# Kernel optimization log

Measured on AMD Instinct MI355X. Metric: run time of the kernel, lower is better.

## Reference

```python
import jax, jax.numpy as jnp
import numpy as np

U, I, D = 100000, 50000, 64
N = U + I
E_G, E_U, E_I = 2400000, 1600000, 800000


def _spmm(rows, cols, vals, x, n):
    # sparse [n, m] @ dense [m, d] via gather + scale + segment-sum scatter
    return jax.ops.segment_sum(x[cols] * vals[:, None], rows, num_segments=n)


def setup_inputs() -> dict:
    key = jax.random.key(0)
    ks = jax.random.split(key, 11)
    return {
        "user_emb": jax.random.normal(ks[0], (U, D), dtype=jnp.float32),
        "item_emb": jax.random.normal(ks[1], (I, D), dtype=jnp.float32),
        "graph_rows": jax.random.randint(ks[2], (E_G,), 0, N, dtype=jnp.int32),
        "graph_cols": jax.random.randint(ks[3], (E_G,), 0, N, dtype=jnp.int32),
        "graph_vals": jax.random.uniform(ks[4], (E_G,), dtype=jnp.float32),
        "user_rows": jax.random.randint(ks[5], (E_U,), 0, U, dtype=jnp.int32),
        "user_cols": jax.random.randint(ks[6], (E_U,), 0, U, dtype=jnp.int32),
        "user_vals": jax.random.uniform(ks[7], (E_U,), dtype=jnp.float32),
        "item_rows": jax.random.randint(ks[8], (E_I,), 0, I, dtype=jnp.int32),
        "item_cols": jax.random.randint(ks[9], (E_I,), 0, I, dtype=jnp.int32),
        "item_vals": jax.random.uniform(ks[10], (E_I,), dtype=jnp.float32),
    }


def reference(user_emb, item_emb,
              graph_rows, graph_cols, graph_vals,
              user_rows, user_cols, user_vals,
              item_rows, item_cols, item_vals):
    all_emb = jnp.concatenate([user_emb, item_emb], axis=0)  # [N, D]
    all_emb1 = _spmm(graph_rows, graph_cols, graph_vals, all_emb, N)
    user_emb2 = _spmm(user_rows, user_cols, user_vals, user_emb, U)
    item_emb2 = _spmm(item_rows, item_cols, item_vals, item_emb, I)
    user_emb1, item_emb1 = all_emb1[:U], all_emb1[U:]
    return (user_emb1, item_emb1, user_emb2, item_emb2)
```

## Files before the change

kernel.cpp:

```cpp
#include <hip/hip_runtime.h>

#define DDIM 64
constexpr int U_CNT = 100000;
constexpr int I_CNT = 50000;
constexpr int N_CNT = U_CNT + I_CNT;
constexpr int NB    = N_CNT + U_CNT + I_CNT;

constexpr int BIN_ROWS_LOG = 8;
constexpr int BIN_ROWS = 1 << BIN_ROWS_LOG;
constexpr int BINS = (NB + BIN_ROWS - 1) / BIN_ROWS;
constexpr int BINS_PAD = 1536;
constexpr int SORT_EDGES = 4096;
constexpr int HIST_EDGES = 16384;
constexpr int CAP = 4672;
constexpr int NSLOT = 10;

constexpr int SB_LOG = 12;
constexpr int NSB = (NB + (1 << SB_LOG) - 1) >> SB_LOG;
constexpr int NSB_PAD = 128;
constexpr int BWIN = 48;

typedef unsigned u32x2 __attribute__((ext_vector_type(2)));
typedef unsigned u32x4 __attribute__((ext_vector_type(4)));

__device__ __forceinline__ int wave_incl_scan(int v, int lane) {
#pragma unroll
    for (int off = 1; off < 64; off <<= 1) {
        int t = __shfl_up(v, off, 64);
        if (lane >= off) v += t;
    }
    return v;
}

__device__ __forceinline__ unsigned short f2bf_rne(float f) {
    unsigned u = __float_as_uint(f);
    unsigned r = (u + 0x7FFFu + ((u >> 16) & 1u)) >> 16;
    return (unsigned short)r;
}

__global__ __launch_bounds__(256) void convert_emb(const float* __restrict__ ue,
                                                   const float* __restrict__ ie,
                                                   unsigned short* __restrict__ emb16) {
    int g = blockIdx.x * 256 + threadIdx.x;
    constexpr int UG = U_CNT * (DDIM / 4);
    constexpr int TG = N_CNT * (DDIM / 4);
    if (g >= TG) return;
    float4 v = (g < UG) ? ((const float4*)ue)[g] : ((const float4*)ie)[g - UG];
    ushort4 o;
    o.x = f2bf_rne(v.x); o.y = f2bf_rne(v.y); o.z = f2bf_rne(v.z); o.w = f2bf_rne(v.w);
    ((ushort4*)emb16)[g] = o;
}

__global__ __launch_bounds__(1024) void hist_conv(const int* __restrict__ gr,
                                                  const int* __restrict__ ur,
                                                  const int* __restrict__ ir,
                                                  int EG, int EU, int EI,
                                                  int* __restrict__ cnt,
                                                  const float* __restrict__ ue,
                                                  const float* __restrict__ ie,
                                                  unsigned short* __restrict__ emb16) {
    __shared__ int h[BINS_PAD];
    for (int i = threadIdx.x; i < BINS_PAD; i += 1024) h[i] = 0;

    if (emb16) {
        constexpr int UG = U_CNT * (DDIM / 4);
        constexpr int TG = N_CNT * (DDIM / 4);
        int stride = (int)gridDim.x * 1024;
        for (int g = blockIdx.x * 1024 + threadIdx.x; g < TG; g += stride) {
            float4 v = (g < UG) ? ((const float4*)ue)[g] : ((const float4*)ie)[g - UG];
            ushort4 o;
            o.x = f2bf_rne(v.x); o.y = f2bf_rne(v.y); o.z = f2bf_rne(v.z); o.w = f2bf_rne(v.w);
            ((ushort4*)emb16)[g] = o;
        }
    }
    __syncthreads();

    int base = blockIdx.x * HIST_EDGES;
    int Et = EG + EU + EI;
    for (int j = 0; j < HIST_EDGES / 1024; ++j) {
        int e = base + j * 1024 + threadIdx.x;
        if (e < Et) {
            int b;
            if (e < EG)           b = gr[e];
            else if (e < EG + EU) b = N_CNT + ur[e - EG];
            else                  b = N_CNT + U_CNT + ir[e - EG - EU];
            atomicAdd(&h[b >> BIN_ROWS_LOG], 1);
        }
    }
    __syncthreads();
    for (int i = threadIdx.x; i < BINS; i += 1024) {
        int v = h[i];
        if (v) atomicAdd(&cnt[i], v);
    }
}

__global__ __launch_bounds__(1024) void scan_bins(const int* __restrict__ cnt,
                                                  int* __restrict__ bin_base,
                                                  int* __restrict__ bin_cursor,
                                                  int* __restrict__ sb_base,
                                                  int* __restrict__ sb_cursor,
                                                  int E_total) {
    __shared__ int wsum[16], woff[16];
    int tid = threadIdx.x, lane = tid & 63, wid = tid >> 6;
    int i0 = 2 * tid, i1 = 2 * tid + 1;
    int c0 = (i0 < BINS) ? cnt[i0] : 0;
    int c1 = (i1 < BINS) ? cnt[i1] : 0;
    int v = c0 + c1;
    int incl = wave_incl_scan(v, lane);
    if (lane == 63) wsum[wid] = incl;
    __syncthreads();
    if (wid == 0 && lane < 16) {
        int s = wsum[lane], si = s;
#pragma unroll
        for (int off = 1; off < 16; off <<= 1) {
            int t = __shfl_up(si, off, 64);
            if (lane >= off) si += t;
        }
        woff[lane] = si - s;
    }
    __syncthreads();
    int e = incl - v + woff[wid];
    if (i0 < BINS) { bin_base[i0] = e;      bin_cursor[i0] = e; }
    if (i1 < BINS) { bin_base[i1] = e + c0; bin_cursor[i1] = e + c0; }
    if (tid == 0) bin_base[BINS] = E_total;
    if (sb_base) {
        __syncthreads();
        if (tid <= NSB) {
            int idx = tid << (SB_LOG - BIN_ROWS_LOG);
            int vv = (idx >= BINS) ? E_total : bin_base[idx];
            sb_base[tid] = vv;
            if (tid < NSB) sb_cursor[tid] = vv;
        }
    }
}

__global__ __launch_bounds__(512, 6) void sbsort_all(
        const int* __restrict__ gr, const int* __restrict__ gc, const float* __restrict__ gv,
        const int* __restrict__ ur, const int* __restrict__ uc, const float* __restrict__ uv,
        const int* __restrict__ ir, const int* __restrict__ ic, const float* __restrict__ iv,
        int EG, int EU, int EI,
        int* __restrict__ sb_cursor, uint2* __restrict__ poolA) {
    __shared__ uint2 sorted[SORT_EDGES];
    __shared__ unsigned char ssb[SORT_EDGES];
    __shared__ int hist[NSB_PAD];
    __shared__ int lscan[NSB_PAD];
    __shared__ int lcur[NSB_PAD];
    __shared__ int wsum2[2];

    int tid = threadIdx.x, lane = tid & 63, wid = tid >> 6;
    for (int i = tid; i < NSB_PAD; i += 512) { hist[i] = 0; lcur[i] = 0; }
    __syncthreads();

    const int Et = EG + EU + EI;
    int start = blockIdx.x * SORT_EDGES;
    int base_e = start + tid * 8;
    int myb[8]; unsigned mylo[8]; float myv[8];

#pragma unroll
    for (int j = 0; j < 8; j += 4) {
        int e = base_e + j;
        int sg0 = (e < EG) ? 0 : (e < EG + EU ? 1 : 2);
        int sg3 = (e + 3 < EG) ? 0 : (e + 3 < EG + EU ? 1 : 2);
        if (e + 3 < Et && sg0 == sg3) {
            const int* R; const int* Cc; const float* V; int boff, goff, loc;
            if (sg0 == 0)      { R = gr; Cc = gc; V = gv; boff = 0;             goff = 0;     loc = e; }
            else if (sg0 == 1) { R = ur; Cc = uc; V = uv; boff = N_CNT;         goff = 0;     loc = e - EG; }
            else               { R = ir; Cc = ic; V = iv; boff = N_CNT + U_CNT; goff = U_CNT; loc = e - EG - EU; }
            int4   r4 = *(const int4*)(R + loc);
            int4   c4 = *(const int4*)(Cc + loc);
            float4 v4 = *(const float4*)(V + loc);
            int rr[4] = {r4.x, r4.y, r4.z, r4.w};
            int cc[4] = {c4.x, c4.y, c4.z, c4.w};
            float vv[4] = {v4.x, v4.y, v4.z, v4.w};
#pragma unroll
            for (int q = 0; q < 4; ++q) {
                int bucket = boff + rr[q];
                int sb = bucket >> SB_LOG;
                myb[j + q] = sb;
                mylo[j + q] = ((unsigned)(bucket & 4095) << 18) | (unsigned)(goff + cc[q]);
                myv[j + q] = vv[q];
                atomicAdd(&hist[sb], 1);
            }
        } else {
#pragma unroll
            for (int q = 0; q < 4; ++q) {
                int ee = e + q;
                if (ee < Et) {
                    int r, c; float vl; int boff, goff;
                    if (ee < EG)           { r = gr[ee]; c = gc[ee]; vl = gv[ee]; boff = 0; goff = 0; }
                    else if (ee < EG + EU) { int k = ee - EG;      r = ur[k]; c = uc[k]; vl = uv[k]; boff = N_CNT;         goff = 0; }
                    else                   { int k = ee - EG - EU; r = ir[k]; c = ic[k]; vl = iv[k]; boff = N_CNT + U_CNT; goff = U_CNT; }
                    int bucket = boff + r;
                    int sb = bucket >> SB_LOG;
                    myb[j + q] = sb;
                    mylo[j + q] = ((unsigned)(bucket & 4095) << 18) | (unsigned)(goff + c);
                    myv[j + q] = vl;
                    atomicAdd(&hist[sb], 1);
                } else myb[j + q] = -1;
            }
        }
    }
    __syncthreads();

    int v = 0, incl = 0;
    if (tid < NSB_PAD) {
        v = hist[tid];
        incl = wave_incl_scan(v, lane);
        if (lane == 63) wsum2[wid] = incl;
    }
    __syncthreads();
    if (tid < NSB_PAD) {
        int st = incl - v + (wid ? wsum2[0] : 0);
        lscan[tid] = st;
        if (tid < NSB && v) hist[tid] = atomicAdd(&sb_cursor[tid], v);
    }
    __syncthreads();

#pragma unroll
    for (int j = 0; j < 8; ++j) {
        if (myb[j] >= 0) {
            int p = lscan[myb[j]] + atomicAdd(&lcur[myb[j]], 1);
            sorted[p] = make_uint2(mylo[j], __float_as_uint(myv[j]));
            ssb[p] = (unsigned char)myb[j];
        }
    }
    __syncthreads();

    int cntE = min(SORT_EDGES, Et - start);
    for (int pos = tid; pos < cntE; pos += 512) {
        int b = ssb[pos];
        uint2 t = sorted[pos];
        u32x2 q; q.x = t.x; q.y = t.y;
        __builtin_nontemporal_store(q, (u32x2*)&poolA[hist[b] + (pos - lscan[b])]);
    }
}

__global__ __launch_bounds__(512, 6) void binsort2(const uint2* __restrict__ poolA,
                                                   const int* __restrict__ sb_base, int Et,
                                                   int* __restrict__ bin_cursor,
                                                   uint2* __restrict__ poolB) {
    __shared__ uint2 sorted[SORT_EDGES];
    __shared__ unsigned char sbin[SORT_EDGES];
    __shared__ int hist[BWIN];
    __shared__ int lscan[BWIN];
    __shared__ int lcur[BWIN];
    __shared__ int ssbb[NSB + 1];
    __shared__ int W0s, nloc;

    int tid = threadIdx.x, lane = tid & 63;
    if (tid < BWIN) { hist[tid] = 0; }
    if (tid <= NSB) ssbb[tid] = sb_base[tid];
    __syncthreads();

    int start = blockIdx.x * SORT_EDGES;
    int base_e = start + tid * 8;
    int sb;
    {
        int lo2 = 0, hi2 = NSB - 1;
        while (lo2 < hi2) {
            int mid = (lo2 + hi2 + 1) >> 1;
            if (ssbb[mid] <= base_e) lo2 = mid; else hi2 = mid - 1;
        }
        sb = lo2;
    }
    if (tid == 0) W0s = sb << (SB_LOG - BIN_ROWS_LOG);
    __syncthreads();
    int W0 = W0s;

    int myb[8]; uint2 myp[8];
#pragma unroll
    for (int j = 0; j < 8; j += 2) {
        int e = base_e + j;
        uint2 p0, p1;
        bool v1 = (e + 1 < Et), v0 = (e < Et);
        if (v1) {
            u32x4 q = __builtin_nontemporal_load((const u32x4*)(poolA + e));
            p0.x = q.x; p0.y = q.y; p1.x = q.z; p1.y = q.w;
        } else if (v0) {
            u32x2 q = __builtin_nontemporal_load((const u32x2*)(poolA + e));
            p0.x = q.x; p0.y = q.y;
        }
        if (v0) {
            while (sb < NSB - 1 && e >= ssbb[sb + 1]) ++sb;
            int b = (sb << (SB_LOG - BIN_ROWS_LOG)) + (int)(p0.x >> 26);
            int slot = b - W0;
            if ((unsigned)slot < (unsigned)BWIN) {
                myb[j] = slot; myp[j] = p0;
                atomicAdd(&hist[slot], 1);
            } else {
                int gp = atomicAdd(&bin_cursor[b], 1);
                poolB[gp] = p0;
                myb[j] = -1;
            }
        } else myb[j] = -1;
        if (v1) {
            int e1 = e + 1;
            while (sb < NSB - 1 && e1 >= ssbb[sb + 1]) ++sb;
            int b = (sb << (SB_LOG - BIN_ROWS_LOG)) + (int)(p1.x >> 26);
            int slot = b - W0;
            if ((unsigned)slot < (unsigned)BWIN) {
                myb[j + 1] = slot; myp[j + 1] = p1;
                atomicAdd(&hist[slot], 1);
            } else {
                int gp = atomicAdd(&bin_cursor[b], 1);
                poolB[gp] = p1;
                myb[j + 1] = -1;
            }
        } else myb[j + 1] = -1;
    }
    __syncthreads();

    if (tid < 64) {
        int vv = (tid < BWIN) ? hist[tid] : 0;
        int incl = wave_incl_scan(vv, lane);
        if (tid < BWIN) { lscan[tid] = incl - vv; lcur[tid] = incl - vv; }
        if (tid == BWIN - 1) nloc = incl;
    }
    __syncthreads();
    if (tid < BWIN && hist[tid] > 0)
        hist[tid] = atomicAdd(&bin_cursor[W0 + tid], hist[tid]);
    __syncthreads();

#pragma unroll
    for (int j = 0; j < 8; ++j) {
        if (myb[j] >= 0) {
            int p = atomicAdd(&lcur[myb[j]], 1);
            sorted[p] = myp[j];
            sbin[p] = (unsigned char)myb[j];
        }
    }
    __syncthreads();

    int tot = nloc;
    for (int pos = tid; pos < tot; pos += 512) {
        int sl = sbin[pos];
        uint2 t = sorted[pos];
        u32x2 q; q.x = t.x; q.y = t.y;
        __builtin_nontemporal_store(q, (u32x2*)&poolB[hist[sl] + (pos - lscan[sl])]);
    }
}

__global__ __launch_bounds__(512) void binsort(const int* __restrict__ rows,
                                               const int* __restrict__ cols,
                                               const float* __restrict__ vals, int E,
                                               int bucket_base, int gidx_base,
                                               int* __restrict__ bin_cursor,
                                               uint2* __restrict__ pool) {
    __shared__ uint2 sorted[SORT_EDGES];
    __shared__ unsigned short sbin[SORT_EDGES];
    __shared__ int hist[BINS_PAD];
    __shared__ int lscan[BINS_PAD];
    __shared__ int lcur[BINS_PAD];
    __shared__ int wsum[8], woff[8];

    int tid = threadIdx.x, lane = tid & 63, wid = tid >> 6;
    for (int i = tid; i < BINS_PAD; i += 512) { hist[i] = 0; lcur[i] = 0; }
    __syncthreads();

    int start = blockIdx.x * SORT_EDGES;
    int base_e = start + tid * 8;
    int myb[8]; unsigned mylo[8]; float myv[8];
#pragma unroll
    for (int j = 0; j < 8; j += 4) {
        int e = base_e + j;
        if (e + 3 < E) {
            int4   r4 = *(const int4*)(rows + e);
            int4   c4 = *(const int4*)(cols + e);
            float4 v4 = *(const float4*)(vals + e);
            int rr[4] = {r4.x, r4.y, r4.z, r4.w};
            int cc[4] = {c4.x, c4.y, c4.z, c4.w};
            float vv[4] = {v4.x, v4.y, v4.z, v4.w};
#pragma unroll
            for (int q = 0; q < 4; ++q) {
                int bucket = bucket_base + rr[q];
                myb[j + q] = bucket >> BIN_ROWS_LOG;
                mylo[j + q] = ((unsigned)(bucket & (BIN_ROWS - 1)) << 18) |
                              (unsigned)(gidx_base + cc[q]);
                myv[j + q] = vv[q];
                atomicAdd(&hist[myb[j + q]], 1);
            }
        } else {
#pragma unroll
            for (int q = 0; q < 4; ++q) {
                int ee = e + q;
                if (ee < E) {
                    int bucket = bucket_base + rows[ee];
                    myb[j + q] = bucket >> BIN_ROWS_LOG;
                    mylo[j + q] = ((unsigned)(bucket & (BIN_ROWS - 1)) << 18) |
                                  (unsigned)(gidx_base + cols[ee]);
                    myv[j + q] = vals[ee];
                    atomicAdd(&hist[myb[j + q]], 1);
                } else myb[j + q] = -1;
            }
        }
    }
    __syncthreads();

    int s0 = 3 * tid, s1 = s0 + 1, s2 = s0 + 2;
    int h0 = hist[s0], h1 = hist[s1], h2 = hist[s2];
    int v = h0 + h1 + h2;
    int incl = wave_incl_scan(v, lane);
    if (lane == 63) wsum[wid] = incl;
    __syncthreads();
    if (wid == 0 && lane < 8) {
        int s = wsum[lane], si = s;
#pragma unroll
        for (int off = 1; off < 8; off <<= 1) {
            int t = __shfl_up(si, off, 64);
            if (lane >= off) si += t;
        }
        woff[lane] = si - s;
    }
    __syncthreads();
    int e0 = incl - v + woff[wid];
    lscan[s0] = e0; lscan[s1] = e0 + h0; lscan[s2] = e0 + h0 + h1;
    if (s0 < BINS && h0) hist[s0] = atomicAdd(&bin_cursor[s0], h0);
    if (s1 < BINS && h1) hist[s1] = atomicAdd(&bin_cursor[s1], h1);
    if (s2 < BINS && h2) hist[s2] = atomicAdd(&bin_cursor[s2], h2);
    __syncthreads();

#pragma unroll
    for (int j = 0; j < 8; ++j) {
        if (myb[j] >= 0) {
            int p = lscan[myb[j]] + atomicAdd(&lcur[myb[j]], 1);
            sorted[p] = make_uint2(mylo[j], __float_as_uint(myv[j]));
            sbin[p] = (unsigned short)myb[j];
        }
    }
    __syncthreads();

    int cntE = min(SORT_EDGES, E - start);
    for (int pos = tid; pos < cntE; pos += 512) {
        int b = sbin[pos];
        pool[hist[b] + (pos - lscan[b])] = sorted[pos];
    }
}

template <bool BF16>
__global__ __launch_bounds__(512, 8) void refine_accum(const int* __restrict__ bin_base,
                                                       const uint2* __restrict__ pool,
                                                       const unsigned short* __restrict__ emb16,
                                                       const float* __restrict__ ue,
                                                       const float* __restrict__ ie,
                                                       float* __restrict__ out) {
    __shared__ uint2 sorted[CAP];
    __shared__ int rhist[BIN_ROWS];
    __shared__ int rstart[BIN_ROWS];
    __shared__ int rcur[BIN_ROWS];
    __shared__ int wsum[4];
    int tid = threadIdx.x, lane = tid & 63, wid = tid >> 6;
    int b = blockIdx.x;
    int s = bin_base[b], e = bin_base[b + 1];
    int cnt = min(e - s, CAP);

    if (tid < BIN_ROWS) rhist[tid] = 0;
    __syncthreads();

    uint2 my[NSLOT];
    const u32x2* poolv = (const u32x2*)(pool + s);
#pragma unroll
    for (int j = 0; j < NSLOT; ++j) {
        int idx = tid + j * 512;
        if (idx < cnt) {
            u32x2 q = __builtin_nontemporal_load(poolv + idx);
            my[j].x = q.x; my[j].y = q.y;
            atomicAdd(&rhist[(q.x >> 18) & 255u], 1);
        }
    }
    __syncthreads();

    int v = 0, incl = 0;
    if (tid < BIN_ROWS) {
        v = rhist[tid];
        incl = wave_incl_scan(v, lane);
        if (lane == 63) wsum[wid] = incl;
    }
    __syncthreads();
    if (tid < BIN_ROWS) {
        int off = 0;
#pragma unroll
        for (int w = 0; w < 4; ++w)
            if (w < wid) off += wsum[w];
        int st = incl - v + off;
        rstart[tid] = st; rcur[tid] = st;
    }
    __syncthreads();

#pragma unroll
    for (int j = 0; j < NSLOT; ++j) {
        int idx = tid + j * 512;
        if (idx < cnt) {
            int pos = atomicAdd(&rcur[(my[j].x >> 18) & 255u], 1);
            sorted[pos] = my[j];
        }
    }
    __syncthreads();

    long long rowbase = (long long)b * BIN_ROWS;
    auto gather = [&](unsigned gi) -> float {
        if (BF16) return __uint_as_float((unsigned)emb16[(gi << 6) + lane] << 16);
        return (gi < (unsigned)U_CNT) ? ue[((size_t)gi << 6) + lane]
                                      : ie[(((size_t)gi - U_CNT) << 6) + lane];
    };
    for (int r = wid; r < BIN_ROWS; r += 8) {
        long long row = rowbase + r;
        if (row >= NB) break;
        int k = rstart[r], ke = k + rhist[r];
        float acc0 = 0.f, acc1 = 0.f;
        for (; k + 8 <= ke; k += 8) {
            uint2 p0 = sorted[k],     p1 = sorted[k + 1], p2 = sorted[k + 2], p3 = sorted[k + 3];
            uint2 p4 = sorted[k + 4], p5 = sorted[k + 5], p6 = sorted[k + 6], p7 = sorted[k + 7];
            float x0 = gather(p0.x & 0x3FFFFu);
            float x1 = gather(p1.x & 0x3FFFFu);
            float x2 = gather(p2.x & 0x3FFFFu);
            float x3 = gather(p3.x & 0x3FFFFu);
            float x4 = gather(p4.x & 0x3FFFFu);
            float x5 = gather(p5.x & 0x3FFFFu);
            float x6 = gather(p6.x & 0x3FFFFu);
            float x7 = gather(p7.x & 0x3FFFFu);
            acc0 += __uint_as_float(p0.y) * x0;
            acc1 += __uint_as_float(p1.y) * x1;
            acc0 += __uint_as_float(p2.y) * x2;
            acc1 += __uint_as_float(p3.y) * x3;
            acc0 += __uint_as_float(p4.y) * x4;
            acc1 += __uint_as_float(p5.y) * x5;
            acc0 += __uint_as_float(p6.y) * x6;
            acc1 += __uint_as_float(p7.y) * x7;
        }
        for (; k + 4 <= ke; k += 4) {
            uint2 p0 = sorted[k], p1 = sorted[k + 1], p2 = sorted[k + 2], p3 = sorted[k + 3];
            float x0 = gather(p0.x & 0x3FFFFu);
            float x1 = gather(p1.x & 0x3FFFFu);
            float x2 = gather(p2.x & 0x3FFFFu);
            float x3 = gather(p3.x & 0x3FFFFu);
            acc0 += __uint_as_float(p0.y) * x0;
            acc1 += __uint_as_float(p1.y) * x1;
            acc0 += __uint_as_float(p2.y) * x2;
            acc1 += __uint_as_float(p3.y) * x3;
        }
        for (; k < ke; ++k) {
            uint2 p = sorted[k];
            acc0 += __uint_as_float(p.y) * gather(p.x & 0x3FFFFu);
        }
        __builtin_nontemporal_store(acc0 + acc1, &out[(size_t)row * DDIM + lane]);
    }
}

__global__ void spmm_graph_kernel(const int* __restrict__ rows, const int* __restrict__ cols,
                                  const float* __restrict__ vals,
                                  const float* __restrict__ user_emb,
                                  const float* __restrict__ item_emb,
                                  float* __restrict__ out, int E) {
    long long idx = (long long)blockIdx.x * blockDim.x + threadIdx.x;
    int e = (int)(idx >> 6), d = (int)(idx & 63);
    if (e >= E) return;
    int r = rows[e], c = cols[e];
    float v = vals[e];
    float x = (c < U_CNT) ? user_emb[(long long)c * DDIM + d]
                          : item_emb[(long long)(c - U_CNT) * DDIM + d];
    atomicAdd(&out[(long long)r * DDIM + d], v * x);
}

__global__ void spmm_plain_kernel(const int* __restrict__ rows, const int* __restrict__ cols,
                                  const float* __restrict__ vals,
                                  const float* __restrict__ emb,
                                  float* __restrict__ out, int E) {
    long long idx = (long long)blockIdx.x * blockDim.x + threadIdx.x;
    int e = (int)(idx >> 6), d = (int)(idx & 63);
    if (e >= E) return;
    int r = rows[e], c = cols[e];
    atomicAdd(&out[(long long)r * DDIM + d], vals[e] * emb[(long long)c * DDIM + d]);
}

extern "C" void kernel_launch(void* const* d_in, const int* in_sizes, int n_in,
                              void* d_out, int out_size, void* d_ws, size_t ws_size,
                              hipStream_t stream) {
    const float* user_emb = (const float*)d_in[0];
    const float* item_emb = (const float*)d_in[1];
    const int*   g_rows   = (const int*)d_in[2];
    const int*   g_cols   = (const int*)d_in[3];
    const float* g_vals   = (const float*)d_in[4];
    const int*   u_rows   = (const int*)d_in[5];
    const int*   u_cols   = (const int*)d_in[6];
    const float* u_vals   = (const float*)d_in[7];
    const int*   i_rows   = (const int*)d_in[8];
    const int*   i_cols   = (const int*)d_in[9];
    const float* i_vals   = (const float*)d_in[10];
    float* out = (float*)d_out;

    const int EG = in_sizes[2];
    const int EU = in_sizes[5];
    const int EI = in_sizes[8];
    const int Et = EG + EU + EI;

    const size_t emb_bytes = (size_t)N_CNT * DDIM * sizeof(unsigned short);

    size_t t_off_bb   = (size_t)BINS_PAD * sizeof(int);
    size_t t_off_bc   = t_off_bb + (size_t)(BINS + 1) * sizeof(int);
    size_t t_off_sbb  = t_off_bc + (size_t)BINS * sizeof(int);
    size_t t_off_sbc  = t_off_sbb + (size_t)(NSB + 1) * sizeof(int);
    size_t t_off_pa   = (t_off_sbc + (size_t)NSB * sizeof(int) + 15) & ~(size_t)15;
    size_t t_off_pb   = t_off_pa + (size_t)Et * sizeof(uint2);
    size_t needed_2p  = t_off_pb + (size_t)Et * sizeof(uint2);
    size_t t_off_emb  = (needed_2p + 15) & ~(size_t)15;
    size_t needed_na  = t_off_emb + emb_bytes;
    bool pa_fits_emb  = (size_t)Et * sizeof(uint2) >= emb_bytes;

    size_t o_off_base   = (size_t)BINS_PAD * sizeof(int);
    size_t o_off_cursor = o_off_base + (size_t)(BINS + 1) * sizeof(int);
    size_t o_off_pool   = (o_off_cursor + (size_t)BINS * sizeof(int) + 15) & ~(size_t)15;
    size_t o_off_emb    = o_off_pool + (size_t)Et * sizeof(uint2);
    size_t needed_min   = o_off_emb;
    size_t needed_full  = o_off_emb + emb_bytes;

    if (ws_size >= needed_2p && pa_fits_emb) {
        bool noalias = (ws_size >= needed_na);
        int*   cnt        = (int*)d_ws;
        int*   bin_base   = (int*)((char*)d_ws + t_off_bb);
        int*   bin_cursor = (int*)((char*)d_ws + t_off_bc);
        int*   sb_base    = (int*)((char*)d_ws + t_off_sbb);
        int*   sb_cursor  = (int*)((char*)d_ws + t_off_sbc);
        uint2* poolA      = (uint2*)((char*)d_ws + t_off_pa);
        uint2* poolB      = (uint2*)((char*)d_ws + t_off_pb);
        unsigned short* emb16 = noalias ? (unsigned short*)((char*)d_ws + t_off_emb)
                                        : (unsigned short*)poolA;

        hipMemsetAsync(cnt, 0, (size_t)BINS_PAD * sizeof(int), stream);

        unsigned hblocks = (unsigned)((Et + HIST_EDGES - 1) / HIST_EDGES);
        hist_conv<<<hblocks, 1024, 0, stream>>>(g_rows, u_rows, i_rows, EG, EU, EI, cnt,
                                                user_emb, item_emb,
                                                noalias ? emb16 : (unsigned short*)nullptr);
        scan_bins<<<1, 1024, 0, stream>>>(cnt, bin_base, bin_cursor, sb_base, sb_cursor, Et);

        unsigned nb2 = (unsigned)((Et + SORT_EDGES - 1) / SORT_EDGES);
        sbsort_all<<<nb2, 512, 0, stream>>>(g_rows, g_cols, g_vals,
                                            u_rows, u_cols, u_vals,
                                            i_rows, i_cols, i_vals,
                                            EG, EU, EI, sb_cursor, poolA);
        binsort2<<<nb2, 512, 0, stream>>>(poolA, sb_base, Et, bin_cursor, poolB);

        if (!noalias) {
            unsigned cgrid = (unsigned)((N_CNT * (DDIM / 4) + 255) / 256);
            convert_emb<<<cgrid, 256, 0, stream>>>(user_emb, item_emb, emb16);
        }

        refine_accum<true><<<BINS, 512, 0, stream>>>(bin_base, poolB, emb16,
                                                     user_emb, item_emb, out);
    } else if (ws_size >= needed_min) {
        int*   cnt        = (int*)d_ws;
        int*   bin_base   = (int*)((char*)d_ws + o_off_base);
        int*   bin_cursor = (int*)((char*)d_ws + o_off_cursor);
        uint2* pool       = (uint2*)((char*)d_ws + o_off_pool);
        unsigned short* emb16 = (unsigned short*)((char*)d_ws + o_off_emb);
        bool use_bf16 = (ws_size >= needed_full);

        hipMemsetAsync(cnt, 0, (size_t)BINS_PAD * sizeof(int), stream);

        unsigned hblocks = (unsigned)((Et + HIST_EDGES - 1) / HIST_EDGES);
        hist_conv<<<hblocks, 1024, 0, stream>>>(g_rows, u_rows, i_rows, EG, EU, EI, cnt,
                                                user_emb, item_emb,
                                                use_bf16 ? emb16 : (unsigned short*)nullptr);
        scan_bins<<<1, 1024, 0, stream>>>(cnt, bin_base, bin_cursor, nullptr, nullptr, Et);

        unsigned gb = (unsigned)((EG + SORT_EDGES - 1) / SORT_EDGES);
        unsigned ub = (unsigned)((EU + SORT_EDGES - 1) / SORT_EDGES);
        unsigned ib = (unsigned)((EI + SORT_EDGES - 1) / SORT_EDGES);
        binsort<<<gb, 512, 0, stream>>>(g_rows, g_cols, g_vals, EG, 0,             0,     bin_cursor, pool);
        binsort<<<ub, 512, 0, stream>>>(u_rows, u_cols, u_vals, EU, N_CNT,         0,     bin_cursor, pool);
        binsort<<<ib, 512, 0, stream>>>(i_rows, i_cols, i_vals, EI, N_CNT + U_CNT, U_CNT, bin_cursor, pool);

        if (use_bf16)
            refine_accum<true><<<BINS, 512, 0, stream>>>(bin_base, pool, emb16,
                                                         user_emb, item_emb, out);
        else
            refine_accum<false><<<BINS, 512, 0, stream>>>(bin_base, pool, (const unsigned short*)nullptr,
                                                          user_emb, item_emb, out);
    } else {
        hipMemsetAsync(d_out, 0, (size_t)out_size * sizeof(float), stream);
        const int block = 256;
        {
            long long t = (long long)EG * DDIM;
            spmm_graph_kernel<<<(unsigned)((t + block - 1) / block), block, 0, stream>>>(
                g_rows, g_cols, g_vals, user_emb, item_emb, out, EG);
        }
        {
            long long t = (long long)EU * DDIM;
            spmm_plain_kernel<<<(unsigned)((t + block - 1) / block), block, 0, stream>>>(
                u_rows, u_cols, u_vals, user_emb, out + (size_t)N_CNT * DDIM, EU);
        }
        {
            long long t = (long long)EI * DDIM;
            spmm_plain_kernel<<<(unsigned)((t + block - 1) / block), block, 0, stream>>>(
                i_rows, i_cols, i_vals, item_emb, out + (size_t)(N_CNT + U_CNT) * DDIM, EI);
        }
    }
}
```

Before: 357.0 us.

## Halve bin size and gather bf16 pairs with half-wave edge split in accumulate

Bins now hold 128 rows instead of 256. The refine kernel drops to 256 threads with a smaller LDS buffer and higher occupancy, and the second-level sort window grows to 80 slots using a two-wave scan. In the accumulate loop each half-wave handles a different edge and loads 32-bit pairs of bf16 values, then the two halves are combined with a cross-half shuffle and written as float2. This aims to cut LDS pressure and use wider gather loads per lane. The fallback one-pass sort path and the fp32 gather path are removed, so small workspaces now go to the naive kernels.

Result: no change. 355.4 us (-0.4%).

```diff
diff --git a/kernel.cpp b/kernel.cpp
--- a/kernel.cpp
+++ b/kernel.cpp
@@ -6,22 +6,24 @@
 constexpr int N_CNT = U_CNT + I_CNT;
 constexpr int NB    = N_CNT + U_CNT + I_CNT;
 
-constexpr int BIN_ROWS_LOG = 8;
+constexpr int BIN_ROWS_LOG = 7;
 constexpr int BIN_ROWS = 1 << BIN_ROWS_LOG;
 constexpr int BINS = (NB + BIN_ROWS - 1) / BIN_ROWS;
-constexpr int BINS_PAD = 1536;
+constexpr int BINS_PAD = 2560;
 constexpr int SORT_EDGES = 4096;
 constexpr int HIST_EDGES = 16384;
-constexpr int CAP = 4672;
+constexpr int CAP = 2432;
 constexpr int NSLOT = 10;
 
 constexpr int SB_LOG = 12;
 constexpr int NSB = (NB + (1 << SB_LOG) - 1) >> SB_LOG;
 constexpr int NSB_PAD = 128;
-constexpr int BWIN = 48;
+constexpr int BWIN = 80;
+constexpr int BWIN_PAD = 128;
 
 typedef unsigned u32x2 __attribute__((ext_vector_type(2)));
 typedef unsigned u32x4 __attribute__((ext_vector_type(4)));
+typedef float    f32x2 __attribute__((ext_vector_type(2)));
 
 __device__ __forceinline__ int wave_incl_scan(int v, int lane) {
 #pragma unroll
@@ -102,10 +104,11 @@
                                                   int E_total) {
     __shared__ int wsum[16], woff[16];
     int tid = threadIdx.x, lane = tid & 63, wid = tid >> 6;
-    int i0 = 2 * tid, i1 = 2 * tid + 1;
+    int i0 = 3 * tid, i1 = i0 + 1, i2 = i0 + 2;
     int c0 = (i0 < BINS) ? cnt[i0] : 0;
     int c1 = (i1 < BINS) ? cnt[i1] : 0;
-    int v = c0 + c1;
+    int c2 = (i2 < BINS) ? cnt[i2] : 0;
+    int v = c0 + c1 + c2;
     int incl = wave_incl_scan(v, lane);
     if (lane == 63) wsum[wid] = incl;
     __syncthreads();
@@ -120,21 +123,20 @@
     }
     __syncthreads();
     int e = incl - v + woff[wid];
-    if (i0 < BINS) { bin_base[i0] = e;      bin_cursor[i0] = e; }
-    if (i1 < BINS) { bin_base[i1] = e + c0; bin_cursor[i1] = e + c0; }
+    if (i0 < BINS) { bin_base[i0] = e;           bin_cursor[i0] = e; }
+    if (i1 < BINS) { bin_base[i1] = e + c0;      bin_cursor[i1] = e + c0; }
+    if (i2 < BINS) { bin_base[i2] = e + c0 + c1; bin_cursor[i2] = e + c0 + c1; }
     if (tid == 0) bin_base[BINS] = E_total;
-    if (sb_base) {
-        __syncthreads();
-        if (tid <= NSB) {
-            int idx = tid << (SB_LOG - BIN_ROWS_LOG);
-            int vv = (idx >= BINS) ? E_total : bin_base[idx];
-            sb_base[tid] = vv;
-            if (tid < NSB) sb_cursor[tid] = vv;
-        }
-    }
-}
-
-__global__ __launch_bounds__(512, 6) void sbsort_all(
+    __syncthreads();
+    if (tid <= NSB) {
+        int idx = tid << (SB_LOG - BIN_ROWS_LOG);
+        int vv = (idx >= BINS) ? E_total : bin_base[idx];
+        sb_base[tid] = vv;
+        if (tid < NSB) sb_cursor[tid] = vv;
+    }
+}
+
+__global__ __launch_bounds__(512, 8) void sbsort_all(
         const int* __restrict__ gr, const int* __restrict__ gc, const float* __restrict__ gv,
         const int* __restrict__ ur, const int* __restrict__ uc, const float* __restrict__ uv,
         const int* __restrict__ ir, const int* __restrict__ ic, const float* __restrict__ iv,
@@ -235,20 +237,21 @@
     }
 }
 
-__global__ __launch_bounds__(512, 6) void binsort2(const uint2* __restrict__ poolA,
+__global__ __launch_bounds__(512, 8) void binsort2(const uint2* __restrict__ poolA,
                                                    const int* __restrict__ sb_base, int Et,
                                                    int* __restrict__ bin_cursor,
                                                    uint2* __restrict__ poolB) {
     __shared__ uint2 sorted[SORT_EDGES];
     __shared__ unsigned char sbin[SORT_EDGES];
-    __shared__ int hist[BWIN];
-    __shared__ int lscan[BWIN];
-    __shared__ int lcur[BWIN];
+    __shared__ int hist[BWIN_PAD];
+    __shared__ int lscan[BWIN_PAD];
+    __shared__ int lcur[BWIN_PAD];
     __shared__ int ssbb[NSB + 1];
-    __shared__ int W0s, nloc;
-
-    int tid = threadIdx.x, lane = tid & 63;
-    if (tid < BWIN) { hist[tid] = 0; }
+    __shared__ int wsum2[2];
+    __shared__ int sblo_s, nloc;
+
+    int tid = threadIdx.x, lane = tid & 63, wid = tid >> 6;
+    if (tid < BWIN_PAD) hist[tid] = 0;
     if (tid <= NSB) ssbb[tid] = sb_base[tid];
     __syncthreads();
 
@@ -263,9 +266,17 @@
         }
         sb = lo2;
     }
-    if (tid == 0) W0s = sb << (SB_LOG - BIN_ROWS_LOG);
-    __syncthreads();
-    int W0 = W0s;
+    if (tid == 0) {
+        int lo2 = 0, hi2 = NSB - 1;
+        while (lo2 < hi2) {
+            int mid = (lo2 + hi2 + 1) >> 1;
+            if (ssbb[mid] <= start) lo2 = mid; else hi2 = mid - 1;
+        }
+        sblo_s = lo2;
+    }
+    __syncthreads();
+    int sb_lo = sblo_s;
+    int W0 = sb_lo << (SB_LOG - BIN_ROWS_LOG);
 
     int myb[8]; uint2 myp[8];
 #pragma unroll
@@ -282,12 +293,12 @@
         }
         if (v0) {
             while (sb < NSB - 1 && e >= ssbb[sb + 1]) ++sb;
-            int b = (sb << (SB_LOG - BIN_ROWS_LOG)) + (int)(p0.x >> 26);
-            int slot = b - W0;
+            int slot = ((sb - sb_lo) << (SB_LOG - BIN_ROWS_LOG)) + (int)(p0.x >> 25);
             if ((unsigned)slot < (unsigned)BWIN) {
                 myb[j] = slot; myp[j] = p0;
                 atomicAdd(&hist[slot], 1);
             } else {
+                int b = (sb << (SB_LOG - BIN_ROWS_LOG)) + (int)(p0.x >> 25);
                 int gp = atomicAdd(&bin_cursor[b], 1);
                 poolB[gp] = p0;
                 myb[j] = -1;
@@ -296,12 +307,12 @@
         if (v1) {
             int e1 = e + 1;
             while (sb < NSB - 1 && e1 >= ssbb[sb + 1]) ++sb;
-            int b = (sb << (SB_LOG - BIN_ROWS_LOG)) + (int)(p1.x >> 26);
-            int slot = b - W0;
+            int slot = ((sb - sb_lo) << (SB_LOG - BIN_ROWS_LOG)) + (int)(p1.x >> 25);
             if ((unsigned)slot < (unsigned)BWIN) {
                 myb[j + 1] = slot; myp[j + 1] = p1;
                 atomicAdd(&hist[slot], 1);
             } else {
+                int b = (sb << (SB_LOG - BIN_ROWS_LOG)) + (int)(p1.x >> 25);
                 int gp = atomicAdd(&bin_cursor[b], 1);
                 poolB[gp] = p1;
                 myb[j + 1] = -1;
@@ -310,11 +321,17 @@
     }
     __syncthreads();
 
-    if (tid < 64) {
-        int vv = (tid < BWIN) ? hist[tid] : 0;
-        int incl = wave_incl_scan(vv, lane);
-        if (tid < BWIN) { lscan[tid] = incl - vv; lcur[tid] = incl - vv; }
-        if (tid == BWIN - 1) nloc = incl;
+    int v = 0, incl = 0;
+    if (tid < BWIN_PAD) {
+        v = hist[tid];
+        incl = wave_incl_scan(v, lane);
+        if (lane == 63) wsum2[wid] = incl;
+    }
+    __syncthreads();
+    if (tid < BWIN_PAD) {
+        int st = incl - v + (wid ? wsum2[0] : 0);
+        lscan[tid] = st; lcur[tid] = st;
+        if (tid == BWIN_PAD - 1) nloc = st + v;
     }
     __syncthreads();
     if (tid < BWIN && hist[tid] > 0)
@@ -340,114 +357,15 @@
     }
 }
 
-__global__ __launch_bounds__(512) void binsort(const int* __restrict__ rows,
-                                               const int* __restrict__ cols,
-                                               const float* __restrict__ vals, int E,
-                                               int bucket_base, int gidx_base,
-                                               int* __restrict__ bin_cursor,
-                                               uint2* __restrict__ pool) {
-    __shared__ uint2 sorted[SORT_EDGES];
-    __shared__ unsigned short sbin[SORT_EDGES];
-    __shared__ int hist[BINS_PAD];
-    __shared__ int lscan[BINS_PAD];
-    __shared__ int lcur[BINS_PAD];
-    __shared__ int wsum[8], woff[8];
-
-    int tid = threadIdx.x, lane = tid & 63, wid = tid >> 6;
-    for (int i = tid; i < BINS_PAD; i += 512) { hist[i] = 0; lcur[i] = 0; }
-    __syncthreads();
-
-    int start = blockIdx.x * SORT_EDGES;
-    int base_e = start + tid * 8;
-    int myb[8]; unsigned mylo[8]; float myv[8];
-#pragma unroll
-    for (int j = 0; j < 8; j += 4) {
-        int e = base_e + j;
-        if (e + 3 < E) {
-            int4   r4 = *(const int4*)(rows + e);
-            int4   c4 = *(const int4*)(cols + e);
-            float4 v4 = *(const float4*)(vals + e);
-            int rr[4] = {r4.x, r4.y, r4.z, r4.w};
-            int cc[4] = {c4.x, c4.y, c4.z, c4.w};
-            float vv[4] = {v4.x, v4.y, v4.z, v4.w};
-#pragma unroll
-            for (int q = 0; q < 4; ++q) {
-                int bucket = bucket_base + rr[q];
-                myb[j + q] = bucket >> BIN_ROWS_LOG;
-                mylo[j + q] = ((unsigned)(bucket & (BIN_ROWS - 1)) << 18) |
-                              (unsigned)(gidx_base + cc[q]);
-                myv[j + q] = vv[q];
-                atomicAdd(&hist[myb[j + q]], 1);
-            }
-        } else {
-#pragma unroll
-            for (int q = 0; q < 4; ++q) {
-                int ee = e + q;
-                if (ee < E) {
-                    int bucket = bucket_base + rows[ee];
-                    myb[j + q] = bucket >> BIN_ROWS_LOG;
-                    mylo[j + q] = ((unsigned)(bucket & (BIN_ROWS - 1)) << 18) |
-                                  (unsigned)(gidx_base + cols[ee]);
-                    myv[j + q] = vals[ee];
-                    atomicAdd(&hist[myb[j + q]], 1);
-                } else myb[j + q] = -1;
-            }
-        }
-    }
-    __syncthreads();
-
-    int s0 = 3 * tid, s1 = s0 + 1, s2 = s0 + 2;
-    int h0 = hist[s0], h1 = hist[s1], h2 = hist[s2];
-    int v = h0 + h1 + h2;
-    int incl = wave_incl_scan(v, lane);
-    if (lane == 63) wsum[wid] = incl;
-    __syncthreads();
-    if (wid == 0 && lane < 8) {
-        int s = wsum[lane], si = s;
-#pragma unroll
-        for (int off = 1; off < 8; off <<= 1) {
-            int t = __shfl_up(si, off, 64);
-            if (lane >= off) si += t;
-        }
-        woff[lane] = si - s;
-    }
-    __syncthreads();
-    int e0 = incl - v + woff[wid];
-    lscan[s0] = e0; lscan[s1] = e0 + h0; lscan[s2] = e0 + h0 + h1;
-    if (s0 < BINS && h0) hist[s0] = atomicAdd(&bin_cursor[s0], h0);
-    if (s1 < BINS && h1) hist[s1] = atomicAdd(&bin_cursor[s1], h1);
-    if (s2 < BINS && h2) hist[s2] = atomicAdd(&bin_cursor[s2], h2);
-    __syncthreads();
-
-#pragma unroll
-    for (int j = 0; j < 8; ++j) {
-        if (myb[j] >= 0) {
-            int p = lscan[myb[j]] + atomicAdd(&lcur[myb[j]], 1);
-            sorted[p] = make_uint2(mylo[j], __float_as_uint(myv[j]));
-            sbin[p] = (unsigned short)myb[j];
-        }
-    }
-    __syncthreads();
-
-    int cntE = min(SORT_EDGES, E - start);
-    for (int pos = tid; pos < cntE; pos += 512) {
-        int b = sbin[pos];
-        pool[hist[b] + (pos - lscan[b])] = sorted[pos];
-    }
-}
-
-template <bool BF16>
-__global__ __launch_bounds__(512, 8) void refine_accum(const int* __restrict__ bin_base,
+__global__ __launch_bounds__(256, 7) void refine_accum(const int* __restrict__ bin_base,
                                                        const uint2* __restrict__ pool,
                                                        const unsigned short* __restrict__ emb16,
-                                                       const float* __restrict__ ue,
-                                                       const float* __restrict__ ie,
                                                        float* __restrict__ out) {
-    __shared__ uint2 sorted[CAP];
+    __shared__ uint2 sorted[CAP + 1];
     __shared__ int rhist[BIN_ROWS];
     __shared__ int rstart[BIN_ROWS];
     __shared__ int rcur[BIN_ROWS];
-    __shared__ int wsum[4];
+    __shared__ int wsum[2];
     int tid = threadIdx.x, lane = tid & 63, wid = tid >> 6;
     int b = blockIdx.x;
     int s = bin_base[b], e = bin_base[b + 1];
@@ -460,11 +378,11 @@
     const u32x2* poolv = (const u32x2*)(pool + s);
 #pragma unroll
     for (int j = 0; j < NSLOT; ++j) {
-        int idx = tid + j * 512;
+        int idx = tid + j * 256;
         if (idx < cnt) {
             u32x2 q = __builtin_nontemporal_load(poolv + idx);
             my[j].x = q.x; my[j].y = q.y;
-            atomicAdd(&rhist[(q.x >> 18) & 255u], 1);
+            atomicAdd(&rhist[(q.x >> 18) & 127u], 1);
         }
     }
     __syncthreads();
@@ -477,72 +395,71 @@
     }
     __syncthreads();
     if (tid < BIN_ROWS) {
-        int off = 0;
-#pragma unroll
-        for (int w = 0; w < 4; ++w)
-            if (w < wid) off += wsum[w];
-        int st = incl - v + off;
+        int st = incl - v + (wid ? wsum[0] : 0);
         rstart[tid] = st; rcur[tid] = st;
     }
     __syncthreads();
 
 #pragma unroll
     for (int j = 0; j < NSLOT; ++j) {
-        int idx = tid + j * 512;
+        int idx = tid + j * 256;
         if (idx < cnt) {
-            int pos = atomicAdd(&rcur[(my[j].x >> 18) & 255u], 1);
+            int pos = atomicAdd(&rcur[(my[j].x >> 18) & 127u], 1);
             sorted[pos] = my[j];
         }
     }
+    if (tid == 0) sorted[cnt] = make_uint2(0u, 0u);
     __syncthreads();
 
     long long rowbase = (long long)b * BIN_ROWS;
-    auto gather = [&](unsigned gi) -> float {
-        if (BF16) return __uint_as_float((unsigned)emb16[(gi << 6) + lane] << 16);
-        return (gi < (unsigned)U_CNT) ? ue[((size_t)gi << 6) + lane]
-                                      : ie[(((size_t)gi - U_CNT) << 6) + lane];
-    };
-    for (int r = wid; r < BIN_ROWS; r += 8) {
+    int half = lane >> 5, hl = lane & 31;
+    const unsigned* emb32 = (const unsigned*)emb16;
+    for (int r = wid; r < BIN_ROWS; r += 4) {
         long long row = rowbase + r;
         if (row >= NB) break;
         int k = rstart[r], ke = k + rhist[r];
-        float acc0 = 0.f, acc1 = 0.f;
+        float a0 = 0.f, a1 = 0.f, c0 = 0.f, c1 = 0.f;
         for (; k + 8 <= ke; k += 8) {
-            uint2 p0 = sorted[k],     p1 = sorted[k + 1], p2 = sorted[k + 2], p3 = sorted[k + 3];
-            uint2 p4 = sorted[k + 4], p5 = sorted[k + 5], p6 = sorted[k + 6], p7 = sorted[k + 7];
-            float x0 = gather(p0.x & 0x3FFFFu);
-            float x1 = gather(p1.x & 0x3FFFFu);
-            float x2 = gather(p2.x & 0x3FFFFu);
-            float x3 = gather(p3.x & 0x3FFFFu);
-            float x4 = gather(p4.x & 0x3FFFFu);
-            float x5 = gather(p5.x & 0x3FFFFu);
-            float x6 = gather(p6.x & 0x3FFFFu);
-            float x7 = gather(p7.x & 0x3FFFFu);
-            acc0 += __uint_as_float(p0.y) * x0;
-            acc1 += __uint_as_float(p1.y) * x1;
-            acc0 += __uint_as_float(p2.y) * x2;
-            acc1 += __uint_as_float(p3.y) * x3;
-            acc0 += __uint_as_float(p4.y) * x4;
-            acc1 += __uint_as_float(p5.y) * x5;
-            acc0 += __uint_as_float(p6.y) * x6;
-            acc1 += __uint_as_float(p7.y) * x7;
-        }
-        for (; k + 4 <= ke; k += 4) {
-            uint2 p0 = sorted[k], p1 = sorted[k + 1], p2 = sorted[k + 2], p3 = sorted[k + 3];
-            float x0 = gather(p0.x & 0x3FFFFu);
-            float x1 = gather(p1.x & 0x3FFFFu);
-            float x2 = gather(p2.x & 0x3FFFFu);
-            float x3 = gather(p3.x & 0x3FFFFu);
-            acc0 += __uint_as_float(p0.y) * x0;
-            acc1 += __uint_as_float(p1.y) * x1;
-            acc0 += __uint_as_float(p2.y) * x2;
-            acc1 += __uint_as_float(p3.y) * x3;
-        }
-        for (; k < ke; ++k) {
-            uint2 p = sorted[k];
-            acc0 += __uint_as_float(p.y) * gather(p.x & 0x3FFFFu);
-        }
-        __builtin_nontemporal_store(acc0 + acc1, &out[(size_t)row * DDIM + lane]);
+            uint2 p0 = sorted[k + half];
+            uint2 p1 = sorted[k + 2 + half];
+            uint2 p2 = sorted[k + 4 + half];
+            uint2 p3 = sorted[k + 6 + half];
+            unsigned w0 = emb32[((size_t)(p0.x & 0x3FFFFu) << 5) + hl];
+            unsigned w1 = emb32[((size_t)(p1.x & 0x3FFFFu) << 5) + hl];
+            unsigned w2 = emb32[((size_t)(p2.x & 0x3FFFFu) << 5) + hl];
+            unsigned w3 = emb32[((size_t)(p3.x & 0x3FFFFu) << 5) + hl];
+            float v0 = __uint_as_float(p0.y), v1 = __uint_as_float(p1.y);
+            float v2 = __uint_as_float(p2.y), v3 = __uint_as_float(p3.y);
+            a0 += v0 * __uint_as_float(w0 << 16);
+            a1 += v0 * __uint_as_float(w0 & 0xFFFF0000u);
+            c0 += v1 * __uint_as_float(w1 << 16);
+            c1 += v1 * __uint_as_float(w1 & 0xFFFF0000u);
+            a0 += v2 * __uint_as_float(w2 << 16);
+            a1 += v2 * __uint_as_float(w2 & 0xFFFF0000u);
+            c0 += v3 * __uint_as_float(w3 << 16);
+            c1 += v3 * __uint_as_float(w3 & 0xFFFF0000u);
+        }
+        for (; k + 2 <= ke; k += 2) {
+            uint2 p = sorted[k + half];
+            unsigned w = emb32[((size_t)(p.x & 0x3FFFFu) << 5) + hl];
+            float v = __uint_as_float(p.y);
+            a0 += v * __uint_as_float(w << 16);
+            a1 += v * __uint_as_float(w & 0xFFFF0000u);
+        }
+        if (k < ke) {
+            uint2 p = sorted[k + half];
+            unsigned w = emb32[((size_t)(p.x & 0x3FFFFu) << 5) + hl];
+            float v = half ? 0.f : __uint_as_float(p.y);
+            a0 += v * __uint_as_float(w << 16);
+            a1 += v * __uint_as_float(w & 0xFFFF0000u);
+        }
+        a0 += c0; a1 += c1;
+        a0 += __shfl_xor(a0, 32, 64);
+        a1 += __shfl_xor(a1, 32, 64);
+        if (lane < 32) {
+            f32x2 o; o.x = a0; o.y = a1;
+            __builtin_nontemporal_store(o, (f32x2*)(out + (size_t)row * DDIM + 2 * hl));
+        }
     }
 }
 
@@ -599,19 +516,12 @@
     size_t t_off_bc   = t_off_bb + (size_t)(BINS + 1) * sizeof(int);
     size_t t_off_sbb  = t_off_bc + (size_t)BINS * sizeof(int);
     size_t t_off_sbc  = t_off_sbb + (size_t)(NSB + 1) * sizeof(int);
-    size_t t_off_pa   = (t_off_sbc + (size_t)NSB * sizeof(int) + 15) & ~(size_t)15;
-    size_t t_off_pb   = t_off_pa + (size_t)Et * sizeof(uint2);
+    size_t t_off_pa   = (t_off_sbc + (size_t)NSB * sizeof(int) + 127) & ~(size_t)127;
+    size_t t_off_pb   = (t_off_pa + (size_t)Et * sizeof(uint2) + 127) & ~(size_t)127;
     size_t needed_2p  = t_off_pb + (size_t)Et * sizeof(uint2);
-    size_t t_off_emb  = (needed_2p + 15) & ~(size_t)15;
+    size_t t_off_emb  = (needed_2p + 127) & ~(size_t)127;
     size_t needed_na  = t_off_emb + emb_bytes;
     bool pa_fits_emb  = (size_t)Et * sizeof(uint2) >= emb_bytes;
-
-    size_t o_off_base   = (size_t)BINS_PAD * sizeof(int);
-    size_t o_off_cursor = o_off_base + (size_t)(BINS + 1) * sizeof(int);
-    size_t o_off_pool   = (o_off_cursor + (size_t)BINS * sizeof(int) + 15) & ~(size_t)15;
-    size_t o_off_emb    = o_off_pool + (size_t)Et * sizeof(uint2);
-    size_t needed_min   = o_off_emb;
-    size_t needed_full  = o_off_emb + emb_bytes;
 
     if (ws_size >= needed_2p && pa_fits_emb) {
         bool noalias = (ws_size >= needed_na);
@@ -645,37 +555,7 @@
             convert_emb<<<cgrid, 256, 0, stream>>>(user_emb, item_emb, emb16);
         }
 
-        refine_accum<true><<<BINS, 512, 0, stream>>>(bin_base, poolB, emb16,
-                                                     user_emb, item_emb, out);
-    } else if (ws_size >= needed_min) {
-        int*   cnt        = (int*)d_ws;
-        int*   bin_base   = (int*)((char*)d_ws + o_off_base);
-        int*   bin_cursor = (int*)((char*)d_ws + o_off_cursor);
-        uint2* pool       = (uint2*)((char*)d_ws + o_off_pool);
-        unsigned short* emb16 = (unsigned short*)((char*)d_ws + o_off_emb);
-        bool use_bf16 = (ws_size >= needed_full);
-
-        hipMemsetAsync(cnt, 0, (size_t)BINS_PAD * sizeof(int), stream);
-
-        unsigned hblocks = (unsigned)((Et + HIST_EDGES - 1) / HIST_EDGES);
-        hist_conv<<<hblocks, 1024, 0, stream>>>(g_rows, u_rows, i_rows, EG, EU, EI, cnt,
-                                                user_emb, item_emb,
-                                                use_bf16 ? emb16 : (unsigned short*)nullptr);
-        scan_bins<<<1, 1024, 0, stream>>>(cnt, bin_base, bin_cursor, nullptr, nullptr, Et);
-
-        unsigned gb = (unsigned)((EG + SORT_EDGES - 1) / SORT_EDGES);
-        unsigned ub = (unsigned)((EU + SORT_EDGES - 1) / SORT_EDGES);
-        unsigned ib = (unsigned)((EI + SORT_EDGES - 1) / SORT_EDGES);
-        binsort<<<gb, 512, 0, stream>>>(g_rows, g_cols, g_vals, EG, 0,             0,     bin_cursor, pool);
-        binsort<<<ub, 512, 0, stream>>>(u_rows, u_cols, u_vals, EU, N_CNT,         0,     bin_cursor, pool);
-        binsort<<<ib, 512, 0, stream>>>(i_rows, i_cols, i_vals, EI, N_CNT + U_CNT, U_CNT, bin_cursor, pool);
-
-        if (use_bf16)
-            refine_accum<true><<<BINS, 512, 0, stream>>>(bin_base, pool, emb16,
-                                                         user_emb, item_emb, out);
-        else
-            refine_accum<false><<<BINS, 512, 0, stream>>>(bin_base, pool, (const unsigned short*)nullptr,
-                                                          user_emb, item_emb, out);
+        refine_accum<<<BINS, 256, 0, stream>>>(bin_base, poolB, emb16, out);
     } else {
         hipMemsetAsync(d_out, 0, (size_t)out_size * sizeof(float), stream);
         const int block = 256;
```
